# Kernel tuning notes

Measured on AMD Instinct MI355X. Metric: run time of the kernel, lower is better.

Reference implementation:

```python
import jax, jax.numpy as jnp
import numpy as np

N_NODES = 100000
N_EDGES = 1000000
IN_CH = 128
HID = 128
N_CLS = 3


def setup_inputs() -> dict:
    key = jax.random.key(0)
    ks = jax.random.split(key, 10)
    scale_in = 1.0 / np.sqrt(IN_CH)
    scale_h = 1.0 / np.sqrt(HID)
    return {
        "x": jax.random.normal(ks[0], (N_NODES, IN_CH), dtype=jnp.float32),
        "edge_index": jax.random.randint(ks[1], (2, N_EDGES), 0, N_NODES, dtype=jnp.int64),
        # SAGEConv layer 1: lin_l (aggregated neighbors, with bias), lin_r (root, no bias)
        "w_l1": jax.random.normal(ks[2], (IN_CH, HID), dtype=jnp.float32) * scale_in,
        "b_l1": jnp.zeros((HID,), dtype=jnp.float32),
        "w_r1": jax.random.normal(ks[3], (IN_CH, HID), dtype=jnp.float32) * scale_in,
        # SAGEConv layer 2
        "w_l2": jax.random.normal(ks[4], (HID, HID), dtype=jnp.float32) * scale_h,
        "b_l2": jnp.zeros((HID,), dtype=jnp.float32),
        "w_r2": jax.random.normal(ks[5], (HID, HID), dtype=jnp.float32) * scale_h,
        # final classifier
        "w_cls": jax.random.normal(ks[6], (HID, N_CLS), dtype=jnp.float32) * scale_h,
        "b_cls": jnp.zeros((N_CLS,), dtype=jnp.float32),
    }


def _sage_conv(x, src, dst, w_l, b_l, w_r, num_nodes):
    # mean aggregation of source-node features onto destination nodes
    msg = x[src]                                              # [E, C] gather
    agg = jax.ops.segment_sum(msg, dst, num_segments=num_nodes)
    cnt = jax.ops.segment_sum(jnp.ones((src.shape[0],), x.dtype), dst,
                              num_segments=num_nodes)
    mean = agg / jnp.maximum(cnt, 1.0)[:, None]
    # out = lin_l(mean_aggr) + lin_r(x)
    return mean @ w_l + b_l + x @ w_r


def reference(x, edge_index, w_l1, b_l1, w_r1, w_l2, b_l2, w_r2, w_cls, b_cls):
    src, dst = edge_index[0], edge_index[1]
    n = x.shape[0]
    h = jax.nn.relu(_sage_conv(x, src, dst, w_l1, b_l1, w_r1, n))
    # dropout is identity in eval mode
    h = jax.nn.relu(_sage_conv(h, src, dst, w_l2, b_l2, w_r2, n))
    logits = h @ w_cls + b_cls
    return logits
```

## Files before the change

kernel.cpp:

```cpp
#include <hip/hip_runtime.h>
#include <hip/hip_bf16.h>

#define N_NODES 100000
#define N_EDGES 1000000
#define CH 128
#define KTOT 256
#define NCLS 3

#define NBKT 196
#define EPB 4096
#define NB_A ((N_EDGES + EPB - 1) / EPB)
#define M_H (NBKT * NB_A)
#define NB_SCAN ((M_H + 1023) / 1024)

#define NB_CVTX (N_NODES * CH / 4 / 256)
#define NB_CVTW (KTOT * CH / 256)
#define NB_A1 (NB_A + NB_CVTX + 2 * NB_CVTW)

typedef __attribute__((ext_vector_type(8))) short v8s;
typedef __attribute__((ext_vector_type(4))) float v4f;

__device__ __forceinline__ float bf2f(unsigned short u) {
    return __uint_as_float(((unsigned int)u) << 16);
}

__device__ __forceinline__ unsigned short f2bf(float f) {
    unsigned int u = __float_as_uint(f);
    unsigned int r = (u + 0x7fffu + ((u >> 16) & 1u)) >> 16;
    return (unsigned short)r;
}

__device__ __forceinline__ int edge_at(const void* e, int is64, long long i) {
    if (is64) return (int)((const long long*)e)[i];
    return ((const int*)e)[i];
}

__device__ __forceinline__ float ldf(const void* p, int isbf, size_t i) {
    if (isbf) return bf2f(((const unsigned short*)p)[i]);
    return ((const float*)p)[i];
}

__device__ __forceinline__ void acc_u32(unsigned int u, float& a0, float& a1) {
    a0 += bf2f((unsigned short)(u & 0xffffu));
    a1 += bf2f((unsigned short)(u >> 16));
}

__global__ void k_init(const void* __restrict__ e, const unsigned int* __restrict__ x,
                       int* __restrict__ eflag, int* __restrict__ dtf,
                       int* __restrict__ done) {
    if (blockIdx.x == 0) {
        if (threadIdx.x < 64) {
            int v = ((const int*)e)[2 * threadIdx.x + 1];
            unsigned long long bl = __ballot(v != 0);
            if (threadIdx.x == 0) *eflag = (bl == 0ULL) ? 1 : 0;
        } else if (threadIdx.x == 64) {
            *done = 0;
        }
    } else {
        if (threadIdx.x < 64) {
            unsigned int u = x[threadIdx.x];
            int ex = (u >> 7) & 0xff;
            int sane = (ex == 0) || (ex >= 100 && ex <= 154);
            unsigned long long bl = __ballot(sane);
            if (threadIdx.x == 0) *dtf = (__popcll(bl) >= 48) ? 1 : 0;
        }
    }
}

__global__ void k_A1(const void* __restrict__ e, const int* __restrict__ eflag,
                     const int* __restrict__ dtf, int* __restrict__ hist,
                     const void* __restrict__ x, unsigned short* __restrict__ Abuf,
                     const void* __restrict__ wl1, const void* __restrict__ wr1,
                     unsigned short* __restrict__ WT1,
                     const void* __restrict__ wl2, const void* __restrict__ wr2,
                     unsigned short* __restrict__ WT2) {
    int b = blockIdx.x;
    int t = threadIdx.x;
    if (b < NB_A) {
        __shared__ int h[NBKT];
        if (t < NBKT) h[t] = 0;
        __syncthreads();
        int is64 = *eflag;
#pragma unroll
        for (int j = 0; j < EPB / 256; j++) {
            int i = b * EPB + j * 256 + t;
            if (i < N_EDGES) {
                int dst = edge_at(e, is64, (long long)N_EDGES + i);
                atomicAdd(&h[dst >> 9], 1);
            }
        }
        __syncthreads();
        if (t < NBKT) hist[t * NB_A + b] = h[t];
    } else {
        int ob = b - NB_A;
        if (ob < NB_CVTX) {
            int idx = ob * 256 + t;
            int node = idx >> 5;
            int ch = (idx & 31) * 4;
            int isbf = *dtf;
            unsigned short o[4];
            if (isbf) {
                ushort4 u = *(const ushort4*)((const unsigned short*)x +
                                              (size_t)node * CH + ch);
                o[0] = u.x; o[1] = u.y; o[2] = u.z; o[3] = u.w;
            } else {
                float4 v = *(const float4*)((const float*)x + (size_t)node * CH + ch);
                o[0] = f2bf(v.x); o[1] = f2bf(v.y); o[2] = f2bf(v.z); o[3] = f2bf(v.w);
            }
            *(ushort4*)(Abuf + (size_t)node * KTOT + CH + ch) =
                make_ushort4(o[0], o[1], o[2], o[3]);
        } else {
            int rel = ob - NB_CVTX;
            const void* wl = (rel < NB_CVTW) ? wl1 : wl2;
            const void* wr = (rel < NB_CVTW) ? wr1 : wr2;
            unsigned short* WT = (rel < NB_CVTW) ? WT1 : WT2;
            int i = (rel % NB_CVTW) * 256 + t;
            int k = i >> 7;
            int n = i & 127;
            int isbf = *dtf;
            float v = (k < CH) ? ldf(wl, isbf, (size_t)k * CH + n)
                               : ldf(wr, isbf, (size_t)(k - CH) * CH + n);
            WT[(size_t)n * KTOT + k] = f2bf(v);
        }
    }
}

__global__ __launch_bounds__(1024) void k_scanH(int* __restrict__ hist,
                                                int* __restrict__ bsum,
                                                int* __restrict__ done) {
    __shared__ int s[1024];
    __shared__ int pre_sh;
    int t = threadIdx.x, b = blockIdx.x;
    int idx = b * 1024 + t;
    int v = (idx < M_H) ? hist[idx] : 0;
    s[t] = v;
    __syncthreads();
    for (int off = 1; off < 1024; off <<= 1) {
        int u = (t >= off) ? s[t - off] : 0;
        __syncthreads();
        s[t] += u;
        __syncthreads();
    }
    if (t == 1023) {
        bsum[b] = s[t];
        __threadfence();
        atomicAdd(done, 1);
    }
    if (t == 0) {
        while (__hip_atomic_load(done, __ATOMIC_ACQUIRE,
                                 __HIP_MEMORY_SCOPE_AGENT) < NB_SCAN) {
        }
        __threadfence();
        int run = 0;
        for (int r = 0; r < b; r++) run += bsum[r];
        pre_sh = run;
    }
    __syncthreads();
    if (idx < M_H) hist[idx] = s[t] - v + pre_sh;
}

__global__ void k_A3(const void* __restrict__ e, const int* __restrict__ eflag,
                     const int* __restrict__ hist, unsigned int* __restrict__ part) {
    __shared__ int cur[NBKT];
    int b = blockIdx.x;
    int t = threadIdx.x;
    if (t < NBKT) cur[t] = hist[t * NB_A + b];
    __syncthreads();
    int is64 = *eflag;
#pragma unroll
    for (int j = 0; j < EPB / 256; j++) {
        int i = b * EPB + j * 256 + t;
        if (i < N_EDGES) {
            int src = edge_at(e, is64, i);
            int dst = edge_at(e, is64, (long long)N_EDGES + i);
            int pos = atomicAdd(&cur[dst >> 9], 1);
            part[pos] = ((unsigned int)src << 9) | (unsigned int)(dst & 511);
        }
    }
}

__global__ __launch_bounds__(1024) void k_B(const int* __restrict__ hist,
                                            const unsigned int* __restrict__ part,
                                            int* __restrict__ row_start,
                                            int* __restrict__ csr_src) {
    __shared__ int dcnt[512], sa[512], curs[512];
    int b = blockIdx.x;
    int t = threadIdx.x;
    int e0 = hist[b * NB_A];
    int e1 = (b + 1 < NBKT) ? hist[(b + 1) * NB_A] : N_EDGES;
    if (t < 512) dcnt[t] = 0;
    __syncthreads();
    for (int i = e0 + t; i < e1; i += 1024)
        atomicAdd(&dcnt[part[i] & 511], 1);
    __syncthreads();
    if (t < 512) sa[t] = dcnt[t];
    __syncthreads();
    for (int off = 1; off < 512; off <<= 1) {
        int v = 0;
        if (t < 512 && t >= off) v = sa[t - off];
        __syncthreads();
        if (t < 512) sa[t] += v;
        __syncthreads();
    }
    if (t < 512) {
        int excl = sa[t] - dcnt[t];
        curs[t] = e0 + excl;
        int node = b * 512 + t;
        if (node < N_NODES) row_start[node] = e0 + excl;
    }
    if (b == 0 && t == 0) row_start[N_NODES] = N_EDGES;
    __syncthreads();
    for (int i = e0 + t; i < e1; i += 1024) {
        unsigned int p = part[i];
        int pos = atomicAdd(&curs[p & 511], 1);
        csr_src[pos] = (int)(p >> 9);
    }
}

__global__ __launch_bounds__(256) void k_agg(
    const int* __restrict__ row_start, const int* __restrict__ csr_src,
    const unsigned short* __restrict__ gsrc, unsigned short* __restrict__ gdst) {
    long long gt = (long long)blockIdx.x * blockDim.x + threadIdx.x;
    int node = (int)(gt >> 4);
    int lane = (int)(gt & 15);
    if (node >= N_NODES) return;
    int beg = row_start[node];
    int end = row_start[node + 1];
    int n = end - beg;
    float a[8];
#pragma unroll
    for (int j = 0; j < 8; j++) a[j] = 0.f;
    if (n > 0) {
        const unsigned short* gbase = gsrc + CH + lane * 8;
        int nm1 = n - 1;
        int s[16];
#pragma unroll
        for (int j = 0; j < 16; j++) {
            int jj = (j < nm1) ? j : nm1;
            s[j] = csr_src[beg + jj];
        }
        uint4 u[16];
#pragma unroll
        for (int j = 0; j < 16; j++)
            u[j] = *(const uint4*)(gbase + (size_t)s[j] * KTOT);
#pragma unroll
        for (int j = 0; j < 16; j++) {
            if (j < n) {
                acc_u32(u[j].x, a[0], a[1]); acc_u32(u[j].y, a[2], a[3]);
                acc_u32(u[j].z, a[4], a[5]); acc_u32(u[j].w, a[6], a[7]);
            }
        }
        int e = beg + 16;
        while (e + 8 <= end) {
            int s2[8];
#pragma unroll
            for (int j = 0; j < 8; j++) s2[j] = csr_src[e + j];
            uint4 u2[8];
#pragma unroll
            for (int j = 0; j < 8; j++)
                u2[j] = *(const uint4*)(gbase + (size_t)s2[j] * KTOT);
#pragma unroll
            for (int j = 0; j < 8; j++) {
                acc_u32(u2[j].x, a[0], a[1]); acc_u32(u2[j].y, a[2], a[3]);
                acc_u32(u2[j].z, a[4], a[5]); acc_u32(u2[j].w, a[6], a[7]);
            }
            e += 8;
        }
        while (e + 2 <= end) {
            int s0 = csr_src[e], s1 = csr_src[e + 1];
            uint4 u0 = *(const uint4*)(gbase + (size_t)s0 * KTOT);
            uint4 u1 = *(const uint4*)(gbase + (size_t)s1 * KTOT);
            acc_u32(u0.x, a[0], a[1]); acc_u32(u0.y, a[2], a[3]);
            acc_u32(u0.z, a[4], a[5]); acc_u32(u0.w, a[6], a[7]);
            acc_u32(u1.x, a[0], a[1]); acc_u32(u1.y, a[2], a[3]);
            acc_u32(u1.z, a[4], a[5]); acc_u32(u1.w, a[6], a[7]);
            e += 2;
        }
        if (e < end) {
            int s0 = csr_src[e];
            uint4 u0 = *(const uint4*)(gbase + (size_t)s0 * KTOT);
            acc_u32(u0.x, a[0], a[1]); acc_u32(u0.y, a[2], a[3]);
            acc_u32(u0.z, a[4], a[5]); acc_u32(u0.w, a[6], a[7]);
        }
    }
    float rinv = 1.0f / (float)max(n, 1);
    unsigned int p0 = (unsigned int)f2bf(a[0] * rinv) | ((unsigned int)f2bf(a[1] * rinv) << 16);
    unsigned int p1 = (unsigned int)f2bf(a[2] * rinv) | ((unsigned int)f2bf(a[3] * rinv) << 16);
    unsigned int p2 = (unsigned int)f2bf(a[4] * rinv) | ((unsigned int)f2bf(a[5] * rinv) << 16);
    unsigned int p3 = (unsigned int)f2bf(a[6] * rinv) | ((unsigned int)f2bf(a[7] * rinv) << 16);
    *(uint4*)(gdst + (size_t)node * KTOT + lane * 8) = make_uint4(p0, p1, p2, p3);
}

#define LDK 40
#define CLS_LD 130
__global__ __launch_bounds__(256) void k_gemm_mfma(
    const unsigned short* __restrict__ Abuf, const unsigned short* __restrict__ WT,
    const void* __restrict__ bias, const int* __restrict__ dtf,
    unsigned short* __restrict__ out, int out_stride, int out_off,
    const void* __restrict__ wcls, const void* __restrict__ bcls,
    float* __restrict__ cls_out) {
    __shared__ unsigned short smem[4 * 128 * LDK];
    __shared__ float wcls_s[CH * NCLS];
    unsigned short* As = smem;
    unsigned short* Bs = smem + 2 * 128 * LDK;
    const int t = threadIdx.x;
    const int w = t >> 6, l = t & 63;
    const int wx = w & 1, wy = w >> 1;
    const int quad = l >> 4, lrow = l & 15;
    const int row0 = blockIdx.x * 128;
    const int srow = t >> 1, shalf = t & 1;
    const int isbf = *dtf;

    if (cls_out) {
        for (int i = t; i < CH * NCLS; i += 256) wcls_s[i] = ldf(wcls, isbf, i);
    }

    int ar = row0 + srow;
    if (ar >= N_NODES) ar = N_NODES - 1;
    const unsigned short* abase = Abuf + (size_t)ar * KTOT + shalf * 16;
    const unsigned short* bbase = WT + (size_t)srow * KTOT + shalf * 16;

    v4f acc[4][4];
#pragma unroll
    for (int i = 0; i < 4; i++)
#pragma unroll
        for (int j = 0; j < 4; j++) acc[i][j] = (v4f){0.f, 0.f, 0.f, 0.f};

    {
        uint4 a0 = *(const uint4*)abase, a1 = *(const uint4*)(abase + 8);
        uint4 b0 = *(const uint4*)bbase, b1 = *(const uint4*)(bbase + 8);
        *(uint4*)&As[srow * LDK + shalf * 16] = a0;
        *(uint4*)&As[srow * LDK + shalf * 16 + 8] = a1;
        *(uint4*)&Bs[srow * LDK + shalf * 16] = b0;
        *(uint4*)&Bs[srow * LDK + shalf * 16 + 8] = b1;
    }
#pragma unroll
    for (int k = 0; k < KTOT / 32; k++) {
        uint4 na0, na1, nb0, nb1;
        if (k < KTOT / 32 - 1) {
            na0 = *(const uint4*)(abase + (k + 1) * 32);
            na1 = *(const uint4*)(abase + (k + 1) * 32 + 8);
            nb0 = *(const uint4*)(bbase + (k + 1) * 32);
            nb1 = *(const uint4*)(bbase + (k + 1) * 32 + 8);
        }
        __syncthreads();
        const int cur = (k & 1) * 128 * LDK, nxt = ((k + 1) & 1) * 128 * LDK;
        v8s af[4], bfr[4];
#pragma unroll
        for (int mi = 0; mi < 4; mi++)
            af[mi] = *(const v8s*)&As[cur + (wy * 64 + mi * 16 + lrow) * LDK + quad * 8];
#pragma unroll
        for (int ni = 0; ni < 4; ni++)
            bfr[ni] = *(const v8s*)&Bs[cur + (wx * 64 + ni * 16 + lrow) * LDK + quad * 8];
#pragma unroll
        for (int mi = 0; mi < 4; mi++)
#pragma unroll
            for (int ni = 0; ni < 4; ni++)
                acc[mi][ni] = __builtin_amdgcn_mfma_f32_16x16x32_bf16(
                    af[mi], bfr[ni], acc[mi][ni], 0, 0, 0);
        if (k < KTOT / 32 - 1) {
            *(uint4*)&As[nxt + srow * LDK + shalf * 16] = na0;
            *(uint4*)&As[nxt + srow * LDK + shalf * 16 + 8] = na1;
            *(uint4*)&Bs[nxt + srow * LDK + shalf * 16] = nb0;
            *(uint4*)&Bs[nxt + srow * LDK + shalf * 16 + 8] = nb1;
        }
    }
    float bj[4];
#pragma unroll
    for (int ni = 0; ni < 4; ni++) bj[ni] = ldf(bias, isbf, wx * 64 + ni * 16 + lrow);

    if (!cls_out) {
#pragma unroll
        for (int mi = 0; mi < 4; mi++) {
#pragma unroll
            for (int r = 0; r < 4; r++) {
                int grow = row0 + wy * 64 + mi * 16 + quad * 4 + r;
                if (grow < N_NODES) {
#pragma unroll
                    for (int ni = 0; ni < 4; ni++) {
                        int col = wx * 64 + ni * 16 + lrow;
                        float v = fmaxf(acc[mi][ni][r] + bj[ni], 0.0f);
                        out[(size_t)grow * out_stride + out_off + col] = f2bf(v);
                    }
                }
            }
        }
    } else {
        __syncthreads();
#pragma unroll
        for (int mi = 0; mi < 4; mi++) {
#pragma unroll
            for (int r = 0; r < 4; r++) {
                int row = wy * 64 + mi * 16 + quad * 4 + r;
#pragma unroll
                for (int ni = 0; ni < 4; ni++) {
                    int col = wx * 64 + ni * 16 + lrow;
                    float v = fmaxf(acc[mi][ni][r] + bj[ni], 0.0f);
                    smem[row * CLS_LD + col] = f2bf(v);
                }
            }
        }
        __syncthreads();
        if (t < 128) {
            int grow = row0 + t;
            if (grow < N_NODES) {
                float a0 = 0.f, a1 = 0.f, a2 = 0.f;
                for (int k = 0; k < CH; k++) {
                    float h = bf2f(smem[t * CLS_LD + k]);
                    a0 += h * wcls_s[k * NCLS + 0];
                    a1 += h * wcls_s[k * NCLS + 1];
                    a2 += h * wcls_s[k * NCLS + 2];
                }
                cls_out[(size_t)grow * NCLS + 0] = a0 + ldf(bcls, isbf, 0);
                cls_out[(size_t)grow * NCLS + 1] = a1 + ldf(bcls, isbf, 1);
                cls_out[(size_t)grow * NCLS + 2] = a2 + ldf(bcls, isbf, 2);
            }
        }
    }
}

extern "C" void kernel_launch(void* const* d_in, const int* in_sizes, int n_in,
                              void* d_out, int out_size, void* d_ws, size_t ws_size,
                              hipStream_t stream) {
    const void* x = d_in[0];
    const void* eidx = d_in[1];
    const void* w_l1 = d_in[2];
    const void* b_l1 = d_in[3];
    const void* w_r1 = d_in[4];
    const void* w_l2 = d_in[5];
    const void* b_l2 = d_in[6];
    const void* w_r2 = d_in[7];
    const void* w_cls = d_in[8];
    const void* b_cls = d_in[9];

    char* w = (char*)d_ws;
    int* eflag = (int*)w;
    int* dtf = (int*)(w + 64);
    int* done = (int*)(w + 128);
    int* hist = (int*)(w + 4096);
    int* bsum = (int*)(w + 196608);
    int* row_start = (int*)(w + 262144);
    unsigned int* part = (unsigned int*)(w + 720896);
    int* csr_src = (int*)(w + 4915200);
    unsigned short* WT1 = (unsigned short*)(w + 8978432);
    unsigned short* WT2 = (unsigned short*)(w + 9043968);
    unsigned short* A1 = (unsigned short*)(w + 11534336);
    unsigned short* A2 = (unsigned short*)(w + 62914560);

    hipLaunchKernelGGL(k_init, dim3(2), dim3(256), 0, stream,
                       eidx, (const unsigned int*)x, eflag, dtf, done);
    hipLaunchKernelGGL(k_A1, dim3(NB_A1), dim3(256), 0, stream,
                       eidx, eflag, dtf, hist, x, A1,
                       w_l1, w_r1, WT1, w_l2, w_r2, WT2);
    hipLaunchKernelGGL(k_scanH, dim3(NB_SCAN), dim3(1024), 0, stream,
                       hist, bsum, done);
    hipLaunchKernelGGL(k_A3, dim3(NB_A), dim3(256), 0, stream,
                       eidx, eflag, hist, part);
    hipLaunchKernelGGL(k_B, dim3(NBKT), dim3(1024), 0, stream,
                       hist, part, row_start, csr_src);
    hipLaunchKernelGGL(k_agg, dim3(N_NODES * 16 / 256), dim3(256), 0, stream,
                       row_start, csr_src, A1, A1);
    hipLaunchKernelGGL(k_gemm_mfma, dim3((N_NODES + 127) / 128), dim3(256), 0, stream,
                       A1, WT1, b_l1, dtf, A2, KTOT, CH,
                       (const void*)nullptr, (const void*)nullptr, (float*)nullptr);
    hipLaunchKernelGGL(k_agg, dim3(N_NODES * 16 / 256), dim3(256), 0, stream,
                       row_start, csr_src, A2, A2);
    hipLaunchKernelGGL(k_gemm_mfma, dim3((N_NODES + 127) / 128), dim3(256), 0, stream,
                       A2, WT2, b_l2, dtf, (unsigned short*)nullptr, 0, 0,
                       w_cls, b_cls, (float*)d_out);
}
```

Baseline: 262.3 us.

## Fuse mean aggregation into the MFMA GEMM via shared-memory A tile

Drops the separate k_agg kernels. Each GEMM block now gathers and averages its own 128 nodes' neighbor rows straight into a shared-memory tile for the first half of K, and streams the root features for the second half. Feature buffers shrink from an interleaved 256-wide layout to compact 128-wide arrays. This removes the global write and re-read of the aggregated features and two launches. The cost is that the gather work is serialized per block ahead of the MFMA loop, and the larger shared-memory footprint may lower occupancy.

```diff
diff --git a/kernel.cpp b/kernel.cpp
--- a/kernel.cpp
+++ b/kernel.cpp
@@ -69,7 +69,7 @@
 
 __global__ void k_A1(const void* __restrict__ e, const int* __restrict__ eflag,
                      const int* __restrict__ dtf, int* __restrict__ hist,
-                     const void* __restrict__ x, unsigned short* __restrict__ Abuf,
+                     const void* __restrict__ x, unsigned short* __restrict__ Xb,
                      const void* __restrict__ wl1, const void* __restrict__ wr1,
                      unsigned short* __restrict__ WT1,
                      const void* __restrict__ wl2, const void* __restrict__ wr2,
@@ -107,7 +107,7 @@
                 float4 v = *(const float4*)((const float*)x + (size_t)node * CH + ch);
                 o[0] = f2bf(v.x); o[1] = f2bf(v.y); o[2] = f2bf(v.z); o[3] = f2bf(v.w);
             }
-            *(ushort4*)(Abuf + (size_t)node * KTOT + CH + ch) =
+            *(ushort4*)(Xb + (size_t)node * CH + ch) =
                 make_ushort4(o[0], o[1], o[2], o[3]);
         } else {
             int rel = ob - NB_CVTX;
@@ -217,89 +217,19 @@
     }
 }
 
-__global__ __launch_bounds__(256) void k_agg(
+#define LDK 40
+#define LDA 136
+#define CLS_LD 130
+__global__ __launch_bounds__(256) void k_gemm_fused(
     const int* __restrict__ row_start, const int* __restrict__ csr_src,
-    const unsigned short* __restrict__ gsrc, unsigned short* __restrict__ gdst) {
-    long long gt = (long long)blockIdx.x * blockDim.x + threadIdx.x;
-    int node = (int)(gt >> 4);
-    int lane = (int)(gt & 15);
-    if (node >= N_NODES) return;
-    int beg = row_start[node];
-    int end = row_start[node + 1];
-    int n = end - beg;
-    float a[8];
-#pragma unroll
-    for (int j = 0; j < 8; j++) a[j] = 0.f;
-    if (n > 0) {
-        const unsigned short* gbase = gsrc + CH + lane * 8;
-        int nm1 = n - 1;
-        int s[16];
-#pragma unroll
-        for (int j = 0; j < 16; j++) {
-            int jj = (j < nm1) ? j : nm1;
-            s[j] = csr_src[beg + jj];
-        }
-        uint4 u[16];
-#pragma unroll
-        for (int j = 0; j < 16; j++)
-            u[j] = *(const uint4*)(gbase + (size_t)s[j] * KTOT);
-#pragma unroll
-        for (int j = 0; j < 16; j++) {
-            if (j < n) {
-                acc_u32(u[j].x, a[0], a[1]); acc_u32(u[j].y, a[2], a[3]);
-                acc_u32(u[j].z, a[4], a[5]); acc_u32(u[j].w, a[6], a[7]);
-            }
-        }
-        int e = beg + 16;
-        while (e + 8 <= end) {
-            int s2[8];
-#pragma unroll
-            for (int j = 0; j < 8; j++) s2[j] = csr_src[e + j];
-            uint4 u2[8];
-#pragma unroll
-            for (int j = 0; j < 8; j++)
-                u2[j] = *(const uint4*)(gbase + (size_t)s2[j] * KTOT);
-#pragma unroll
-            for (int j = 0; j < 8; j++) {
-                acc_u32(u2[j].x, a[0], a[1]); acc_u32(u2[j].y, a[2], a[3]);
-                acc_u32(u2[j].z, a[4], a[5]); acc_u32(u2[j].w, a[6], a[7]);
-            }
-            e += 8;
-        }
-        while (e + 2 <= end) {
-            int s0 = csr_src[e], s1 = csr_src[e + 1];
-            uint4 u0 = *(const uint4*)(gbase + (size_t)s0 * KTOT);
-            uint4 u1 = *(const uint4*)(gbase + (size_t)s1 * KTOT);
-            acc_u32(u0.x, a[0], a[1]); acc_u32(u0.y, a[2], a[3]);
-            acc_u32(u0.z, a[4], a[5]); acc_u32(u0.w, a[6], a[7]);
-            acc_u32(u1.x, a[0], a[1]); acc_u32(u1.y, a[2], a[3]);
-            acc_u32(u1.z, a[4], a[5]); acc_u32(u1.w, a[6], a[7]);
-            e += 2;
-        }
-        if (e < end) {
-            int s0 = csr_src[e];
-            uint4 u0 = *(const uint4*)(gbase + (size_t)s0 * KTOT);
-            acc_u32(u0.x, a[0], a[1]); acc_u32(u0.y, a[2], a[3]);
-            acc_u32(u0.z, a[4], a[5]); acc_u32(u0.w, a[6], a[7]);
-        }
-    }
-    float rinv = 1.0f / (float)max(n, 1);
-    unsigned int p0 = (unsigned int)f2bf(a[0] * rinv) | ((unsigned int)f2bf(a[1] * rinv) << 16);
-    unsigned int p1 = (unsigned int)f2bf(a[2] * rinv) | ((unsigned int)f2bf(a[3] * rinv) << 16);
-    unsigned int p2 = (unsigned int)f2bf(a[4] * rinv) | ((unsigned int)f2bf(a[5] * rinv) << 16);
-    unsigned int p3 = (unsigned int)f2bf(a[6] * rinv) | ((unsigned int)f2bf(a[7] * rinv) << 16);
-    *(uint4*)(gdst + (size_t)node * KTOT + lane * 8) = make_uint4(p0, p1, p2, p3);
-}
-
-#define LDK 40
-#define CLS_LD 130
-__global__ __launch_bounds__(256) void k_gemm_mfma(
-    const unsigned short* __restrict__ Abuf, const unsigned short* __restrict__ WT,
-    const void* __restrict__ bias, const int* __restrict__ dtf,
-    unsigned short* __restrict__ out, int out_stride, int out_off,
+    const unsigned short* __restrict__ src,
+    const unsigned short* __restrict__ WT, const void* __restrict__ bias,
+    const int* __restrict__ dtf,
+    unsigned short* __restrict__ out,
     const void* __restrict__ wcls, const void* __restrict__ bcls,
     float* __restrict__ cls_out) {
     __shared__ unsigned short smem[4 * 128 * LDK];
+    __shared__ unsigned short Am[128 * LDA];
     __shared__ float wcls_s[CH * NCLS];
     unsigned short* As = smem;
     unsigned short* Bs = smem + 2 * 128 * LDK;
@@ -315,9 +245,77 @@
         for (int i = t; i < CH * NCLS; i += 256) wcls_s[i] = ldf(wcls, isbf, i);
     }
 
+    {
+        const int lane = t & 15, nd = t >> 4;
+        const unsigned short* gbase = src + lane * 8;
+#pragma unroll 1
+        for (int p = 0; p < 8; p++) {
+            int nl = p * 16 + nd;
+            int node = row0 + nl;
+            float a[8];
+#pragma unroll
+            for (int j = 0; j < 8; j++) a[j] = 0.f;
+            int n = 0;
+            if (node < N_NODES) {
+                int beg = row_start[node];
+                int end = row_start[node + 1];
+                n = end - beg;
+                if (n > 0) {
+                    int nm1 = n - 1;
+                    int s[16];
+#pragma unroll
+                    for (int j = 0; j < 16; j++) {
+                        int jj = (j < nm1) ? j : nm1;
+                        s[j] = csr_src[beg + jj];
+                    }
+                    uint4 u[16];
+#pragma unroll
+                    for (int j = 0; j < 16; j++)
+                        u[j] = *(const uint4*)(gbase + (size_t)s[j] * CH);
+#pragma unroll
+                    for (int j = 0; j < 16; j++) {
+                        if (j < n) {
+                            acc_u32(u[j].x, a[0], a[1]); acc_u32(u[j].y, a[2], a[3]);
+                            acc_u32(u[j].z, a[4], a[5]); acc_u32(u[j].w, a[6], a[7]);
+                        }
+                    }
+                    int e = beg + 16;
+                    while (e + 8 <= end) {
+                        int s2[8];
+#pragma unroll
+                        for (int j = 0; j < 8; j++) s2[j] = csr_src[e + j];
+                        uint4 u2[8];
+#pragma unroll
+                        for (int j = 0; j < 8; j++)
+                            u2[j] = *(const uint4*)(gbase + (size_t)s2[j] * CH);
+#pragma unroll
+                        for (int j = 0; j < 8; j++) {
+                            acc_u32(u2[j].x, a[0], a[1]); acc_u32(u2[j].y, a[2], a[3]);
+                            acc_u32(u2[j].z, a[4], a[5]); acc_u32(u2[j].w, a[6], a[7]);
+                        }
+                        e += 8;
+                    }
+                    while (e < end) {
+                        int s0 = csr_src[e];
+                        uint4 u0 = *(const uint4*)(gbase + (size_t)s0 * CH);
+                        acc_u32(u0.x, a[0], a[1]); acc_u32(u0.y, a[2], a[3]);
+                        acc_u32(u0.z, a[4], a[5]); acc_u32(u0.w, a[6], a[7]);
+                        e++;
+                    }
+                }
+            }
+            float rinv = 1.0f / (float)max(n, 1);
+            unsigned int p0 = (unsigned int)f2bf(a[0] * rinv) | ((unsigned int)f2bf(a[1] * rinv) << 16);
+            unsigned int p1 = (unsigned int)f2bf(a[2] * rinv) | ((unsigned int)f2bf(a[3] * rinv) << 16);
+            unsigned int p2 = (unsigned int)f2bf(a[4] * rinv) | ((unsigned int)f2bf(a[5] * rinv) << 16);
+            unsigned int p3 = (unsigned int)f2bf(a[6] * rinv) | ((unsigned int)f2bf(a[7] * rinv) << 16);
+            *(uint4*)&Am[nl * LDA + lane * 8] = make_uint4(p0, p1, p2, p3);
+        }
+    }
+
     int ar = row0 + srow;
     if (ar >= N_NODES) ar = N_NODES - 1;
-    const unsigned short* abase = Abuf + (size_t)ar * KTOT + shalf * 16;
+    const unsigned short* abase = src + (size_t)ar * CH + shalf * 16;
     const unsigned short* bbase = WT + (size_t)srow * KTOT + shalf * 16;
 
     v4f acc[4][4];
@@ -327,10 +325,7 @@
         for (int j = 0; j < 4; j++) acc[i][j] = (v4f){0.f, 0.f, 0.f, 0.f};
 
     {
-        uint4 a0 = *(const uint4*)abase, a1 = *(const uint4*)(abase + 8);
         uint4 b0 = *(const uint4*)bbase, b1 = *(const uint4*)(bbase + 8);
-        *(uint4*)&As[srow * LDK + shalf * 16] = a0;
-        *(uint4*)&As[srow * LDK + shalf * 16 + 8] = a1;
         *(uint4*)&Bs[srow * LDK + shalf * 16] = b0;
         *(uint4*)&Bs[srow * LDK + shalf * 16 + 8] = b1;
     }
@@ -338,17 +333,27 @@
     for (int k = 0; k < KTOT / 32; k++) {
         uint4 na0, na1, nb0, nb1;
         if (k < KTOT / 32 - 1) {
-            na0 = *(const uint4*)(abase + (k + 1) * 32);
-            na1 = *(const uint4*)(abase + (k + 1) * 32 + 8);
             nb0 = *(const uint4*)(bbase + (k + 1) * 32);
             nb1 = *(const uint4*)(bbase + (k + 1) * 32 + 8);
+            if (k >= 3) {
+                na0 = *(const uint4*)(abase + (k - 3) * 32);
+                na1 = *(const uint4*)(abase + (k - 3) * 32 + 8);
+            }
         }
         __syncthreads();
         const int cur = (k & 1) * 128 * LDK, nxt = ((k + 1) & 1) * 128 * LDK;
         v8s af[4], bfr[4];
-#pragma unroll
-        for (int mi = 0; mi < 4; mi++)
-            af[mi] = *(const v8s*)&As[cur + (wy * 64 + mi * 16 + lrow) * LDK + quad * 8];
+        if (k < 4) {
+#pragma unroll
+            for (int mi = 0; mi < 4; mi++)
+                af[mi] = *(const v8s*)&Am[(wy * 64 + mi * 16 + lrow) * LDA +
+                                          k * 32 + quad * 8];
+        } else {
+#pragma unroll
+            for (int mi = 0; mi < 4; mi++)
+                af[mi] = *(const v8s*)&As[cur + (wy * 64 + mi * 16 + lrow) * LDK +
+                                          quad * 8];
+        }
 #pragma unroll
         for (int ni = 0; ni < 4; ni++)
             bfr[ni] = *(const v8s*)&Bs[cur + (wx * 64 + ni * 16 + lrow) * LDK + quad * 8];
@@ -359,10 +364,12 @@
                 acc[mi][ni] = __builtin_amdgcn_mfma_f32_16x16x32_bf16(
                     af[mi], bfr[ni], acc[mi][ni], 0, 0, 0);
         if (k < KTOT / 32 - 1) {
-            *(uint4*)&As[nxt + srow * LDK + shalf * 16] = na0;
-            *(uint4*)&As[nxt + srow * LDK + shalf * 16 + 8] = na1;
             *(uint4*)&Bs[nxt + srow * LDK + shalf * 16] = nb0;
             *(uint4*)&Bs[nxt + srow * LDK + shalf * 16 + 8] = nb1;
+            if (k >= 3) {
+                *(uint4*)&As[nxt + srow * LDK + shalf * 16] = na0;
+                *(uint4*)&As[nxt + srow * LDK + shalf * 16 + 8] = na1;
+            }
         }
     }
     float bj[4];
@@ -380,7 +387,7 @@
                     for (int ni = 0; ni < 4; ni++) {
                         int col = wx * 64 + ni * 16 + lrow;
                         float v = fmaxf(acc[mi][ni][r] + bj[ni], 0.0f);
-                        out[(size_t)grow * out_stride + out_off + col] = f2bf(v);
+                        out[(size_t)grow * CH + col] = f2bf(v);
                     }
                 }
             }
@@ -444,13 +451,13 @@
     int* csr_src = (int*)(w + 4915200);
     unsigned short* WT1 = (unsigned short*)(w + 8978432);
     unsigned short* WT2 = (unsigned short*)(w + 9043968);
-    unsigned short* A1 = (unsigned short*)(w + 11534336);
-    unsigned short* A2 = (unsigned short*)(w + 62914560);
+    unsigned short* Xb = (unsigned short*)(w + 11534336);
+    unsigned short* Hb = (unsigned short*)(w + 62914560);
 
     hipLaunchKernelGGL(k_init, dim3(2), dim3(256), 0, stream,
                        eidx, (const unsigned int*)x, eflag, dtf, done);
     hipLaunchKernelGGL(k_A1, dim3(NB_A1), dim3(256), 0, stream,
-                       eidx, eflag, dtf, hist, x, A1,
+                       eidx, eflag, dtf, hist, x, Xb,
                        w_l1, w_r1, WT1, w_l2, w_r2, WT2);
     hipLaunchKernelGGL(k_scanH, dim3(NB_SCAN), dim3(1024), 0, stream,
                        hist, bsum, done);
@@ -458,14 +465,10 @@
                        eidx, eflag, hist, part);
     hipLaunchKernelGGL(k_B, dim3(NBKT), dim3(1024), 0, stream,
                        hist, part, row_start, csr_src);
-    hipLaunchKernelGGL(k_agg, dim3(N_NODES * 16 / 256), dim3(256), 0, stream,
-                       row_start, csr_src, A1, A1);
-    hipLaunchKernelGGL(k_gemm_mfma, dim3((N_NODES + 127) / 128), dim3(256), 0, stream,
-                       A1, WT1, b_l1, dtf, A2, KTOT, CH,
+    hipLaunchKernelGGL(k_gemm_fused, dim3((N_NODES + 127) / 128), dim3(256), 0, stream,
+                       row_start, csr_src, Xb, WT1, b_l1, dtf, Hb,
                        (const void*)nullptr, (const void*)nullptr, (float*)nullptr);
-    hipLaunchKernelGGL(k_agg, dim3(N_NODES * 16 / 256), dim3(256), 0, stream,
-                       row_start, csr_src, A2, A2);
-    hipLaunchKernelGGL(k_gemm_mfma, dim3((N_NODES + 127) / 128), dim3(256), 0, stream,
-                       A2, WT2, b_l2, dtf, (unsigned short*)nullptr, 0, 0,
-                       w_cls, b_cls, (float*)d_out);
-}
+    hipLaunchKernelGGL(k_gemm_fused, dim3((N_NODES + 127) / 128), dim3(256), 0, stream,
+                       row_start, csr_src, Hb, WT2, b_l2, dtf,
+                       (unsigned short*)nullptr, w_cls, b_cls, (float*)d_out);
+}
```

Result: slower. 279.6 us (+6.6%).

## Split interleaved [mean|x] buffer into separate compact node-feature arrays

Applied to the files above, without the earlier changes.

Node features and aggregated means move from one interleaved 256-wide bf16 row into separate dense 128-wide buffers (Xb, Mb, Hb). The gather in k_agg now reads rows of a compact 256-byte-stride array instead of half-rows at a 512-byte stride, which is meant to improve cache-line and TLB locality for the random neighbor reads. The GEMM fetches its K dimension from two base pointers, and the classifier weights now reuse the tile shared memory instead of a separate array, which lowers LDS use. The tail loop of the gather is simplified to process one edge at a time.

```diff
diff --git a/kernel.cpp b/kernel.cpp
--- a/kernel.cpp
+++ b/kernel.cpp
@@ -69,7 +69,7 @@
 
 __global__ void k_A1(const void* __restrict__ e, const int* __restrict__ eflag,
                      const int* __restrict__ dtf, int* __restrict__ hist,
-                     const void* __restrict__ x, unsigned short* __restrict__ Abuf,
+                     const void* __restrict__ x, unsigned short* __restrict__ Xb,
                      const void* __restrict__ wl1, const void* __restrict__ wr1,
                      unsigned short* __restrict__ WT1,
                      const void* __restrict__ wl2, const void* __restrict__ wr2,
@@ -107,7 +107,7 @@
                 float4 v = *(const float4*)((const float*)x + (size_t)node * CH + ch);
                 o[0] = f2bf(v.x); o[1] = f2bf(v.y); o[2] = f2bf(v.z); o[3] = f2bf(v.w);
             }
-            *(ushort4*)(Abuf + (size_t)node * KTOT + CH + ch) =
+            *(ushort4*)(Xb + (size_t)node * CH + ch) =
                 make_ushort4(o[0], o[1], o[2], o[3]);
         } else {
             int rel = ob - NB_CVTX;
@@ -219,7 +219,7 @@
 
 __global__ __launch_bounds__(256) void k_agg(
     const int* __restrict__ row_start, const int* __restrict__ csr_src,
-    const unsigned short* __restrict__ gsrc, unsigned short* __restrict__ gdst) {
+    const unsigned short* __restrict__ src, unsigned short* __restrict__ mdst) {
     long long gt = (long long)blockIdx.x * blockDim.x + threadIdx.x;
     int node = (int)(gt >> 4);
     int lane = (int)(gt & 15);
@@ -231,7 +231,7 @@
 #pragma unroll
     for (int j = 0; j < 8; j++) a[j] = 0.f;
     if (n > 0) {
-        const unsigned short* gbase = gsrc + CH + lane * 8;
+        const unsigned short* gbase = src + lane * 8;
         int nm1 = n - 1;
         int s[16];
 #pragma unroll
@@ -242,7 +242,7 @@
         uint4 u[16];
 #pragma unroll
         for (int j = 0; j < 16; j++)
-            u[j] = *(const uint4*)(gbase + (size_t)s[j] * KTOT);
+            u[j] = *(const uint4*)(gbase + (size_t)s[j] * CH);
 #pragma unroll
         for (int j = 0; j < 16; j++) {
             if (j < n) {
@@ -258,7 +258,7 @@
             uint4 u2[8];
 #pragma unroll
             for (int j = 0; j < 8; j++)
-                u2[j] = *(const uint4*)(gbase + (size_t)s2[j] * KTOT);
+                u2[j] = *(const uint4*)(gbase + (size_t)s2[j] * CH);
 #pragma unroll
             for (int j = 0; j < 8; j++) {
                 acc_u32(u2[j].x, a[0], a[1]); acc_u32(u2[j].y, a[2], a[3]);
@@ -266,21 +266,12 @@
             }
             e += 8;
         }
-        while (e + 2 <= end) {
-            int s0 = csr_src[e], s1 = csr_src[e + 1];
-            uint4 u0 = *(const uint4*)(gbase + (size_t)s0 * KTOT);
-            uint4 u1 = *(const uint4*)(gbase + (size_t)s1 * KTOT);
+        while (e < end) {
+            int s0 = csr_src[e];
+            uint4 u0 = *(const uint4*)(gbase + (size_t)s0 * CH);
             acc_u32(u0.x, a[0], a[1]); acc_u32(u0.y, a[2], a[3]);
             acc_u32(u0.z, a[4], a[5]); acc_u32(u0.w, a[6], a[7]);
-            acc_u32(u1.x, a[0], a[1]); acc_u32(u1.y, a[2], a[3]);
-            acc_u32(u1.z, a[4], a[5]); acc_u32(u1.w, a[6], a[7]);
-            e += 2;
-        }
-        if (e < end) {
-            int s0 = csr_src[e];
-            uint4 u0 = *(const uint4*)(gbase + (size_t)s0 * KTOT);
-            acc_u32(u0.x, a[0], a[1]); acc_u32(u0.y, a[2], a[3]);
-            acc_u32(u0.z, a[4], a[5]); acc_u32(u0.w, a[6], a[7]);
+            e++;
         }
     }
     float rinv = 1.0f / (float)max(n, 1);
@@ -288,19 +279,20 @@
     unsigned int p1 = (unsigned int)f2bf(a[2] * rinv) | ((unsigned int)f2bf(a[3] * rinv) << 16);
     unsigned int p2 = (unsigned int)f2bf(a[4] * rinv) | ((unsigned int)f2bf(a[5] * rinv) << 16);
     unsigned int p3 = (unsigned int)f2bf(a[6] * rinv) | ((unsigned int)f2bf(a[7] * rinv) << 16);
-    *(uint4*)(gdst + (size_t)node * KTOT + lane * 8) = make_uint4(p0, p1, p2, p3);
+    *(uint4*)(mdst + (size_t)node * CH + lane * 8) = make_uint4(p0, p1, p2, p3);
 }
 
 #define LDK 40
 #define CLS_LD 130
 __global__ __launch_bounds__(256) void k_gemm_mfma(
-    const unsigned short* __restrict__ Abuf, const unsigned short* __restrict__ WT,
-    const void* __restrict__ bias, const int* __restrict__ dtf,
-    unsigned short* __restrict__ out, int out_stride, int out_off,
+    const unsigned short* __restrict__ Mb,
+    const unsigned short* __restrict__ Xr,
+    const unsigned short* __restrict__ WT, const void* __restrict__ bias,
+    const int* __restrict__ dtf,
+    unsigned short* __restrict__ out,
     const void* __restrict__ wcls, const void* __restrict__ bcls,
     float* __restrict__ cls_out) {
     __shared__ unsigned short smem[4 * 128 * LDK];
-    __shared__ float wcls_s[CH * NCLS];
     unsigned short* As = smem;
     unsigned short* Bs = smem + 2 * 128 * LDK;
     const int t = threadIdx.x;
@@ -311,13 +303,10 @@
     const int srow = t >> 1, shalf = t & 1;
     const int isbf = *dtf;
 
-    if (cls_out) {
-        for (int i = t; i < CH * NCLS; i += 256) wcls_s[i] = ldf(wcls, isbf, i);
-    }
-
     int ar = row0 + srow;
     if (ar >= N_NODES) ar = N_NODES - 1;
-    const unsigned short* abase = Abuf + (size_t)ar * KTOT + shalf * 16;
+    const unsigned short* abase_m = Mb + (size_t)ar * CH + shalf * 16;
+    const unsigned short* abase_x = Xr + (size_t)ar * CH + shalf * 16;
     const unsigned short* bbase = WT + (size_t)srow * KTOT + shalf * 16;
 
     v4f acc[4][4];
@@ -327,7 +316,7 @@
         for (int j = 0; j < 4; j++) acc[i][j] = (v4f){0.f, 0.f, 0.f, 0.f};
 
     {
-        uint4 a0 = *(const uint4*)abase, a1 = *(const uint4*)(abase + 8);
+        uint4 a0 = *(const uint4*)abase_m, a1 = *(const uint4*)(abase_m + 8);
         uint4 b0 = *(const uint4*)bbase, b1 = *(const uint4*)(bbase + 8);
         *(uint4*)&As[srow * LDK + shalf * 16] = a0;
         *(uint4*)&As[srow * LDK + shalf * 16 + 8] = a1;
@@ -338,8 +327,10 @@
     for (int k = 0; k < KTOT / 32; k++) {
         uint4 na0, na1, nb0, nb1;
         if (k < KTOT / 32 - 1) {
-            na0 = *(const uint4*)(abase + (k + 1) * 32);
-            na1 = *(const uint4*)(abase + (k + 1) * 32 + 8);
+            const unsigned short* na = (k < 3) ? (abase_m + (k + 1) * 32)
+                                               : (abase_x + (k - 3) * 32);
+            na0 = *(const uint4*)na;
+            na1 = *(const uint4*)(na + 8);
             nb0 = *(const uint4*)(bbase + (k + 1) * 32);
             nb1 = *(const uint4*)(bbase + (k + 1) * 32 + 8);
         }
@@ -380,13 +371,15 @@
                     for (int ni = 0; ni < 4; ni++) {
                         int col = wx * 64 + ni * 16 + lrow;
                         float v = fmaxf(acc[mi][ni][r] + bj[ni], 0.0f);
-                        out[(size_t)grow * out_stride + out_off + col] = f2bf(v);
+                        out[(size_t)grow * CH + col] = f2bf(v);
                     }
                 }
             }
         }
     } else {
         __syncthreads();
+        float* wcls_s = (float*)(smem + 16896);
+        for (int i = t; i < CH * NCLS; i += 256) wcls_s[i] = ldf(wcls, isbf, i);
 #pragma unroll
         for (int mi = 0; mi < 4; mi++) {
 #pragma unroll
@@ -444,13 +437,14 @@
     int* csr_src = (int*)(w + 4915200);
     unsigned short* WT1 = (unsigned short*)(w + 8978432);
     unsigned short* WT2 = (unsigned short*)(w + 9043968);
-    unsigned short* A1 = (unsigned short*)(w + 11534336);
-    unsigned short* A2 = (unsigned short*)(w + 62914560);
+    unsigned short* Xb = (unsigned short*)(w + 11534336);
+    unsigned short* Mb = (unsigned short*)(w + 37748736);
+    unsigned short* Hb = (unsigned short*)(w + 67108864);
 
     hipLaunchKernelGGL(k_init, dim3(2), dim3(256), 0, stream,
                        eidx, (const unsigned int*)x, eflag, dtf, done);
     hipLaunchKernelGGL(k_A1, dim3(NB_A1), dim3(256), 0, stream,
-                       eidx, eflag, dtf, hist, x, A1,
+                       eidx, eflag, dtf, hist, x, Xb,
                        w_l1, w_r1, WT1, w_l2, w_r2, WT2);
     hipLaunchKernelGGL(k_scanH, dim3(NB_SCAN), dim3(1024), 0, stream,
                        hist, bsum, done);
@@ -459,13 +453,13 @@
     hipLaunchKernelGGL(k_B, dim3(NBKT), dim3(1024), 0, stream,
                        hist, part, row_start, csr_src);
     hipLaunchKernelGGL(k_agg, dim3(N_NODES * 16 / 256), dim3(256), 0, stream,
-                       row_start, csr_src, A1, A1);
+                       row_start, csr_src, Xb, Mb);
     hipLaunchKernelGGL(k_gemm_mfma, dim3((N_NODES + 127) / 128), dim3(256), 0, stream,
-                       A1, WT1, b_l1, dtf, A2, KTOT, CH,
+                       Mb, Xb, WT1, b_l1, dtf, Hb,
                        (const void*)nullptr, (const void*)nullptr, (float*)nullptr);
     hipLaunchKernelGGL(k_agg, dim3(N_NODES * 16 / 256), dim3(256), 0, stream,
-                       row_start, csr_src, A2, A2);
+                       row_start, csr_src, Hb, Mb);
     hipLaunchKernelGGL(k_gemm_mfma, dim3((N_NODES + 127) / 128), dim3(256), 0, stream,
-                       A2, WT2, b_l2, dtf, (unsigned short*)nullptr, 0, 0,
+                       Mb, Hb, WT2, b_l2, dtf, (unsigned short*)nullptr,
                        w_cls, b_cls, (float*)d_out);
 }
```

Result: faster. 256.1 us (-2.3%).
